# Optimization experiments

Measured on AMD Instinct MI355X. Metric: run time of the kernel, lower is better.

## Reference

```python
import jax, jax.numpy as jnp
import numpy as np

L, DIM, H, DH, MUL = 4, 1024, 16, 64, 4
INNER = H * DH
HID = DIM * MUL
EPS = 1e-5


def setup_inputs() -> dict:
    key = jax.random.key(0)
    ks = jax.random.split(key, 16)
    s = 0.02
    inp = {
        "x": jax.random.normal(ks[0], (2, 2048, DIM), dtype=jnp.float32),
        "ln1_g": jnp.ones((L, DIM), jnp.float32),
        "ln1_b": jnp.zeros((L, DIM), jnp.float32),
        "Wq": jax.random.normal(ks[1], (L, DIM, INNER), jnp.float32) * s,
        "Wk": jax.random.normal(ks[2], (L, DIM, INNER), jnp.float32) * s,
        "Wv": jax.random.normal(ks[3], (L, DIM, INNER), jnp.float32) * s,
        "Wo": jax.random.normal(ks[4], (L, INNER, DIM), jnp.float32) * s,
        "ln3_g": jnp.ones((L, DIM), jnp.float32),
        "ln3_b": jnp.zeros((L, DIM), jnp.float32),
        "fc1_w": jax.random.normal(ks[5], (L, DIM, HID), jnp.float32) * s,
        "fc1_b": jnp.zeros((L, HID), jnp.float32),
        "fc2_w": jax.random.normal(ks[6], (L, HID, DIM), jnp.float32) * s,
        "fc2_b": jnp.zeros((L, DIM), jnp.float32),
    }
    return inp


def _layernorm(x, g, b):
    mu = jnp.mean(x, axis=-1, keepdims=True)
    var = jnp.var(x, axis=-1, keepdims=True)
    return (x - mu) * jax.lax.rsqrt(var + EPS) * g + b


def _attention(xn, wq, wk, wv, wo):
    B, S, _ = xn.shape
    q = (xn @ wq).reshape(B, S, H, DH).transpose(0, 2, 1, 3)  # b h s d
    k = (xn @ wk).reshape(B, S, H, DH).transpose(0, 2, 1, 3)
    v = (xn @ wv).reshape(B, S, H, DH).transpose(0, 2, 1, 3)
    scale = DH ** -0.5
    sim = jnp.einsum("bhid,bhjd->bhij", q, k) * scale
    mask = jnp.triu(jnp.ones((S, S), dtype=bool), k=1)
    sim = jnp.where(mask, jnp.finfo(sim.dtype).min, sim)
    attn = jax.nn.softmax(sim, axis=-1)
    out = jnp.einsum("bhij,bhjd->bhid", attn, v)
    out = out.transpose(0, 2, 1, 3).reshape(B, S, INNER)
    return out @ wo


def reference(x, ln1_g, ln1_b, Wq, Wk, Wv, Wo, ln3_g, ln3_b, fc1_w, fc1_b, fc2_w, fc2_b):
    for l in range(L):
        x = x + _attention(_layernorm(x, ln1_g[l], ln1_b[l]), Wq[l], Wk[l], Wv[l], Wo[l])
        h = _layernorm(x, ln3_g[l], ln3_b[l])
        h = jax.nn.gelu(h @ fc1_w[l] + fc1_b[l], approximate=False)
        x = x + (h @ fc2_w[l] + fc2_b[l])
    return x
```

## Files before the change

### kernel.cpp

```cpp
#include <hip/hip_runtime.h>

typedef unsigned short u16;
typedef unsigned int u32;
typedef __attribute__((ext_vector_type(8))) short short8;
typedef __attribute__((ext_vector_type(4))) float f32x4;
typedef __attribute__((ext_vector_type(4))) unsigned short u16x4;

__device__ inline u16 f2bf(float f) {
  u32 u = __builtin_bit_cast(u32, f);
  u32 r = (u + 0x7fffu + ((u >> 16) & 1u)) >> 16;
  return (u16)r;
}

__device__ inline void gload16(const void* g, void* l) {
  __builtin_amdgcn_global_load_lds((const __attribute__((address_space(1))) void*)g,
                                   (__attribute__((address_space(3))) void*)l, 16, 0, 0);
}

__global__ __launch_bounds__(256) void transpose_cast(
    const float* __restrict__ src, u16* __restrict__ dst, int K, int N)
{
  __shared__ u16 tile[64][72];
  int bk = blockIdx.x * 64, bn = blockIdx.y * 64;
  int t = threadIdx.x;
  int r = t >> 2, c0 = (t & 3) * 16;
  const float* sp = src + (size_t)(bk + r) * N + bn + c0;
#pragma unroll
  for (int j = 0; j < 16; j += 4) {
    float4 v = *(const float4*)(sp + j);
    tile[r][c0 + j + 0] = f2bf(v.x);
    tile[r][c0 + j + 1] = f2bf(v.y);
    tile[r][c0 + j + 2] = f2bf(v.z);
    tile[r][c0 + j + 3] = f2bf(v.w);
  }
  __syncthreads();
  int nr = t >> 2, k0 = (t & 3) * 16;
  u16* dp = dst + (size_t)(bn + nr) * K + bk + k0;
  short8 v0, v1;
#pragma unroll
  for (int j = 0; j < 8; ++j) v0[j] = (short)tile[k0 + j][nr];
#pragma unroll
  for (int j = 0; j < 8; ++j) v1[j] = (short)tile[k0 + 8 + j][nr];
  *(short8*)dp = v0;
  *(short8*)(dp + 8) = v1;
}

__global__ __launch_bounds__(256) void vtranspose(
    const u16* __restrict__ qkv, u16* __restrict__ vtb)
{
  __shared__ u16 tile[64][72];
  int bt = blockIdx.x;
  int bh = blockIdx.y;
  int b = bh >> 4, h = bh & 15;
  const u16* src = qkv + (size_t)b * 2048 * 3072 + 2048 + h * 64;
  u16* dst = vtb + (size_t)bh * 64 * 2048;
  int t = threadIdx.x;
  int r = t >> 2, c0 = (t & 3) * 16;
  const u16* sp = src + (size_t)(bt * 64 + r) * 3072 + c0;
  *(short8*)&tile[r][c0] = *(const short8*)sp;
  *(short8*)&tile[r][c0 + 8] = *(const short8*)(sp + 8);
  __syncthreads();
  int nr = t >> 2, k0 = (t & 3) * 16;
  u16* dp = dst + (size_t)nr * 2048 + bt * 64 + k0;
  short8 v0, v1;
#pragma unroll
  for (int j = 0; j < 8; ++j) v0[j] = (short)tile[k0 + j][nr];
#pragma unroll
  for (int j = 0; j < 8; ++j) v1[j] = (short)tile[k0 + 8 + j][nr];
  *(short8*)dp = v0;
  *(short8*)(dp + 8) = v1;
}

__global__ __launch_bounds__(256) void ln_kernel(
    const float* __restrict__ x, const float* __restrict__ g,
    const float* __restrict__ be, u16* __restrict__ out)
{
  int row = blockIdx.x;
  int t = threadIdx.x;
  const float4* xr = (const float4*)(x + (size_t)row * 1024);
  float4 v = xr[t];
  float s = v.x + v.y + v.z + v.w;
  float ss = v.x * v.x + v.y * v.y + v.z * v.z + v.w * v.w;
#pragma unroll
  for (int off = 1; off < 64; off <<= 1) {
    s += __shfl_xor(s, off);
    ss += __shfl_xor(ss, off);
  }
  __shared__ float red[8];
  int w = t >> 6, lane = t & 63;
  if (lane == 0) { red[w * 2] = s; red[w * 2 + 1] = ss; }
  __syncthreads();
  s = red[0] + red[2] + red[4] + red[6];
  ss = red[1] + red[3] + red[5] + red[7];
  float mu = s * (1.0f / 1024.0f);
  float var = ss * (1.0f / 1024.0f) - mu * mu;
  float rs = rsqrtf(var + 1e-5f);
  float4 gg = ((const float4*)g)[t];
  float4 bb = ((const float4*)be)[t];
  u16x4 o;
  o[0] = f2bf((v.x - mu) * rs * gg.x + bb.x);
  o[1] = f2bf((v.y - mu) * rs * gg.y + bb.y);
  o[2] = f2bf((v.z - mu) * rs * gg.z + bb.z);
  o[3] = f2bf((v.w - mu) * rs * gg.w + bb.w);
  ((u16x4*)(out + (size_t)row * 1024))[t] = o;
}

template <int EPI, int BN>
__global__ __launch_bounds__(256) void gemm_bf16(
    const u16* __restrict__ A, const u16* __restrict__ Bt,
    u16* __restrict__ C, const float* __restrict__ bias, float* X,
    int M, int N, int K)
{
  constexpr int NJ = BN / 32;
  __shared__ __align__(16) u16 As[2][128 * 32];
  __shared__ __align__(16) u16 Bs[2][BN * 32];
  int bm = blockIdx.x * 128, bn = blockIdx.y * BN;
  int klen = K / gridDim.z;
  int kbeg = blockIdx.z * klen;
  int tid = threadIdx.x;
  int w = tid >> 6, lane = tid & 63;
  int wm = (w >> 1) * 64, wn = (w & 1) * (BN / 2);
  int frow = lane & 15, fkb = lane >> 4;

  f32x4 acc[4][NJ];
#pragma unroll
  for (int i = 0; i < 4; ++i)
#pragma unroll
    for (int j = 0; j < NJ; ++j) acc[i][j] = (f32x4){0.f, 0.f, 0.f, 0.f};

  int ca0 = tid, ca1 = tid + 256;
  int ar0 = ca0 >> 2, ak0 = (((ca0 & 3) ^ ((ar0 >> 1) & 3))) * 8;
  int ar1 = ca1 >> 2, ak1 = (((ca1 & 3) ^ ((ar1 >> 1) & 3))) * 8;
  const u16* Abase = A + (size_t)bm * K;
  const u16* Bbase = Bt + (size_t)bn * K;

  int offa[4], offb[NJ];
#pragma unroll
  for (int i = 0; i < 4; ++i) {
    int row = wm + i * 16 + frow;
    offa[i] = row * 32 + ((fkb ^ ((row >> 1) & 3)) * 8);
  }
#pragma unroll
  for (int j = 0; j < NJ; ++j) {
    int row = wn + j * 16 + frow;
    offb[j] = row * 32 + ((fkb ^ ((row >> 1) & 3)) * 8);
  }

  int nt = klen >> 5;

#define STAGE(buf, k0)                                                              \
  do {                                                                              \
    gload16(Abase + (size_t)ar0 * K + (k0) + ak0, &As[buf][(size_t)(w * 64) * 8]);  \
    gload16(Abase + (size_t)ar1 * K + (k0) + ak1, &As[buf][(size_t)(256 + w * 64) * 8]); \
    gload16(Bbase + (size_t)ar0 * K + (k0) + ak0, &Bs[buf][(size_t)(w * 64) * 8]);  \
    if constexpr (BN == 128)                                                        \
      gload16(Bbase + (size_t)ar1 * K + (k0) + ak1, &Bs[buf][(size_t)(256 + w * 64) * 8]); \
  } while (0)

  STAGE(0, kbeg);
  __syncthreads();
  int cur = 0;
  for (int t = 0; t < nt; ++t) {
    if (t + 1 < nt) STAGE(cur ^ 1, kbeg + (t + 1) * 32);
    short8 a[4], b[NJ];
#pragma unroll
    for (int i = 0; i < 4; ++i) a[i] = *(const short8*)&As[cur][offa[i]];
#pragma unroll
    for (int j = 0; j < NJ; ++j) b[j] = *(const short8*)&Bs[cur][offb[j]];
#pragma unroll
    for (int i = 0; i < 4; ++i)
#pragma unroll
      for (int j = 0; j < NJ; ++j)
        acc[i][j] = __builtin_amdgcn_mfma_f32_16x16x32_bf16(a[i], b[j], acc[i][j], 0, 0, 0);
    __syncthreads();
    cur ^= 1;
  }
#undef STAGE

  int r0 = (lane >> 4) * 4;
#pragma unroll
  for (int i = 0; i < 4; ++i) {
#pragma unroll
    for (int r = 0; r < 4; ++r) {
      int gr = bm + wm + i * 16 + r0 + r;
      size_t rowb = (size_t)gr * N;
#pragma unroll
      for (int j = 0; j < NJ; ++j) {
        int gc = bn + wn + j * 16 + frow;
        float v = acc[i][j][r];
        if constexpr (EPI == 0) {
          C[rowb + gc] = f2bf(v);
        } else if constexpr (EPI == 1) {
          v += bias[gc];
          v = 0.5f * v * (1.0f + erff(v * 0.70710678118654752f));
          C[rowb + gc] = f2bf(v);
        } else if constexpr (EPI == 2) {
          if (bias) v += bias[gc];
          X[rowb + gc] += v;
        } else {
          if (kbeg == 0 && bias) v += bias[gc];
          atomicAdd(&X[rowb + gc], v);
        }
      }
    }
  }
}

__global__ __launch_bounds__(256) void flash_attn4(
    const u16* __restrict__ qkv, const u16* __restrict__ vtb, u16* __restrict__ ao)
{
  const int SEQ = 2048, LDQ = 3072;
  const float SCL2 = 0.18033688011112042f;
  int ib = blockIdx.x;
  int qb = (ib < 256) ? (15 - (ib >> 5)) : ((ib - 256) >> 5);
  int bh = ib & 31;
  int b = bh >> 4, h = bh & 15;
  size_t base = (size_t)b * SEQ * LDQ;
  const u16* Qp = qkv + base + h * 64;
  const u16* Kp = qkv + base + 1024 + h * 64;
  const u16* Vtp = vtb + (size_t)bh * 64 * SEQ;

  __shared__ __align__(16) u16 Kt[64][72];
  __shared__ __align__(16) u16 Vt[64][72];
  __shared__ __align__(16) u16 Pl[4][32][72];

  int tid = threadIdx.x;
  int w = tid >> 6, lane = tid & 63;
  int frow = lane & 15, fkh = lane >> 4;
  int fk = fkh * 8;
  int qbase = qb * 128 + w * 32;

  short8 qf[2][2];
#pragma unroll
  for (int qi = 0; qi < 2; ++qi) {
    const u16* qr = Qp + (size_t)(qbase + qi * 16 + frow) * LDQ;
    qf[qi][0] = *(const short8*)(qr + fk);
    qf[qi][1] = *(const short8*)(qr + 32 + fk);
  }

  short8 ones;
#pragma unroll
  for (int j = 0; j < 8; ++j) ones[j] = (short)0x3F80;

  f32x4 o[2][4];
  f32x4 lacc[2];
#pragma unroll
  for (int qi = 0; qi < 2; ++qi) {
    lacc[qi] = (f32x4){0.f, 0.f, 0.f, 0.f};
#pragma unroll
    for (int nf = 0; nf < 4; ++nf) o[qi][nf] = (f32x4){0.f, 0.f, 0.f, 0.f};
  }

  int sr0 = tid >> 3, sc0 = (tid & 7) * 8;
  int sr1 = (tid + 256) >> 3, sc1 = ((tid + 256) & 7) * 8;

  int ntiles = qb * 2 + 2;

  short8 kr0 = *(const short8*)(Kp + (size_t)sr0 * LDQ + sc0);
  short8 kr1 = *(const short8*)(Kp + (size_t)sr1 * LDQ + sc1);
  short8 vr0 = *(const short8*)(Vtp + (size_t)sr0 * SEQ + sc0);
  short8 vr1 = *(const short8*)(Vtp + (size_t)sr1 * SEQ + sc1);

  for (int jb = 0; jb < ntiles; ++jb) {
    __syncthreads();
    *(short8*)&Kt[sr0][sc0] = kr0;
    *(short8*)&Kt[sr1][sc1] = kr1;
    *(short8*)&Vt[sr0][sc0] = vr0;
    *(short8*)&Vt[sr1][sc1] = vr1;
    __syncthreads();

    if (jb + 1 < ntiles) {
      kr0 = *(const short8*)(Kp + (size_t)((jb + 1) * 64 + sr0) * LDQ + sc0);
      kr1 = *(const short8*)(Kp + (size_t)((jb + 1) * 64 + sr1) * LDQ + sc1);
      vr0 = *(const short8*)(Vtp + (size_t)sr0 * SEQ + (jb + 1) * 64 + sc0);
      vr1 = *(const short8*)(Vtp + (size_t)sr1 * SEQ + (jb + 1) * 64 + sc1);
    }

    short8 kf[4][2];
#pragma unroll
    for (int nf = 0; nf < 4; ++nf) {
      kf[nf][0] = *(const short8*)&Kt[nf * 16 + frow][fk];
      kf[nf][1] = *(const short8*)&Kt[nf * 16 + frow][32 + fk];
    }

#pragma unroll
    for (int qi = 0; qi < 2; ++qi) {
      f32x4 s[4];
#pragma unroll
      for (int nf = 0; nf < 4; ++nf) s[nf] = (f32x4){0.f, 0.f, 0.f, 0.f};
#pragma unroll
      for (int nf = 0; nf < 4; ++nf) {
        s[nf] = __builtin_amdgcn_mfma_f32_16x16x32_bf16(qf[qi][0], kf[nf][0], s[nf], 0, 0, 0);
        s[nf] = __builtin_amdgcn_mfma_f32_16x16x32_bf16(qf[qi][1], kf[nf][1], s[nf], 0, 0, 0);
      }

      float pv[4][4];
#pragma unroll
      for (int nf = 0; nf < 4; ++nf)
#pragma unroll
        for (int r = 0; r < 4; ++r) pv[nf][r] = s[nf][r] * SCL2;

      bool needmask = (jb * 64 + 63) > (qbase + qi * 16);
      if (needmask) {
#pragma unroll
        for (int nf = 0; nf < 4; ++nf)
#pragma unroll
          for (int r = 0; r < 4; ++r) {
            int tok = jb * 64 + nf * 16 + frow;
            int qr = qbase + qi * 16 + fkh * 4 + r;
            if (tok > qr) pv[nf][r] = -1e30f;
          }
      }

#pragma unroll
      for (int nf = 0; nf < 4; ++nf)
#pragma unroll
        for (int r = 0; r < 4; ++r) {
          float p = exp2f(pv[nf][r]);
          Pl[w][qi * 16 + fkh * 4 + r][nf * 16 + frow] = f2bf(p);
        }
    }

    asm volatile("s_waitcnt lgkmcnt(0)" ::: "memory");
#pragma unroll
    for (int ks = 0; ks < 2; ++ks) {
      short8 pa0 = *(const short8*)&Pl[w][frow][ks * 32 + fk];
      short8 pa1 = *(const short8*)&Pl[w][16 + frow][ks * 32 + fk];
      lacc[0] = __builtin_amdgcn_mfma_f32_16x16x32_bf16(pa0, ones, lacc[0], 0, 0, 0);
      lacc[1] = __builtin_amdgcn_mfma_f32_16x16x32_bf16(pa1, ones, lacc[1], 0, 0, 0);
#pragma unroll
      for (int nf = 0; nf < 4; ++nf) {
        short8 vb = *(const short8*)&Vt[nf * 16 + frow][ks * 32 + fk];
        o[0][nf] = __builtin_amdgcn_mfma_f32_16x16x32_bf16(pa0, vb, o[0][nf], 0, 0, 0);
        o[1][nf] = __builtin_amdgcn_mfma_f32_16x16x32_bf16(pa1, vb, o[1][nf], 0, 0, 0);
      }
    }
  }

#pragma unroll
  for (int qi = 0; qi < 2; ++qi) {
#pragma unroll
    for (int nf = 0; nf < 4; ++nf) {
#pragma unroll
      for (int r = 0; r < 4; ++r) {
        int qr = qbase + qi * 16 + fkh * 4 + r;
        int dc = nf * 16 + frow;
        ao[((size_t)b * SEQ + qr) * 1024 + h * 64 + dc] = f2bf(o[qi][nf][r] / lacc[qi][r]);
      }
    }
  }
}

extern "C" void kernel_launch(void* const* d_in, const int* in_sizes, int n_in,
                              void* d_out, int out_size, void* d_ws, size_t ws_size,
                              hipStream_t stream)
{
  const float* x_in = (const float*)d_in[0];
  const float* ln1g = (const float*)d_in[1];
  const float* ln1b = (const float*)d_in[2];
  const float* Wq   = (const float*)d_in[3];
  const float* Wk   = (const float*)d_in[4];
  const float* Wv   = (const float*)d_in[5];
  const float* Wo   = (const float*)d_in[6];
  const float* ln3g = (const float*)d_in[7];
  const float* ln3b = (const float*)d_in[8];
  const float* fc1w = (const float*)d_in[9];
  const float* fc1b = (const float*)d_in[10];
  const float* fc2w = (const float*)d_in[11];
  const float* fc2b = (const float*)d_in[12];

  float* xbuf = (float*)d_out;

  char* ws = (char*)d_ws;
  size_t off = 0;
  u16* xn     = (u16*)(ws + off);  off += (size_t)4096 * 1024 * 2;
  u16* qkvb   = (u16*)(ws + off);  off += (size_t)4096 * 3072 * 2;
  u16* aob    = (u16*)(ws + off);  off += (size_t)4096 * 1024 * 2;
  u16* hbuf   = qkvb;
  u16* vtb    = (u16*)(ws + off);  off += (size_t)32 * 64 * 2048 * 2;
  u16* wqkv_l = (u16*)(ws + off);  off += (size_t)3072 * 1024 * 2;
  u16* wo_l   = (u16*)(ws + off);  off += (size_t)1024 * 1024 * 2;
  u16* wfc1_l = (u16*)(ws + off);  off += (size_t)4096 * 1024 * 2;
  u16* wfc2_l = (u16*)(ws + off);  off += (size_t)1024 * 4096 * 2;

  hipMemcpyAsync(xbuf, x_in, (size_t)4096 * 1024 * 4, hipMemcpyDeviceToDevice, stream);

  dim3 blk(256);
  for (int l = 0; l < 4; ++l) {
    transpose_cast<<<dim3(16, 16), blk, 0, stream>>>(Wq + (size_t)l * 1024 * 1024, wqkv_l,                        1024, 1024);
    transpose_cast<<<dim3(16, 16), blk, 0, stream>>>(Wk + (size_t)l * 1024 * 1024, wqkv_l + (size_t)1024 * 1024,  1024, 1024);
    transpose_cast<<<dim3(16, 16), blk, 0, stream>>>(Wv + (size_t)l * 1024 * 1024, wqkv_l + (size_t)2048 * 1024,  1024, 1024);
    transpose_cast<<<dim3(16, 16), blk, 0, stream>>>(Wo + (size_t)l * 1024 * 1024, wo_l,                          1024, 1024);
    transpose_cast<<<dim3(16, 64), blk, 0, stream>>>(fc1w + (size_t)l * 1024 * 4096, wfc1_l,                      1024, 4096);
    transpose_cast<<<dim3(64, 16), blk, 0, stream>>>(fc2w + (size_t)l * 4096 * 1024, wfc2_l,                      4096, 1024);

    ln_kernel<<<4096, blk, 0, stream>>>(xbuf, ln1g + l * 1024, ln1b + l * 1024, xn);
    gemm_bf16<0, 128><<<dim3(32, 24), blk, 0, stream>>>(xn, wqkv_l, qkvb, nullptr, nullptr, 4096, 3072, 1024);
    vtranspose<<<dim3(32, 32), blk, 0, stream>>>(qkvb, vtb);
    flash_attn4<<<dim3(512), blk, 0, stream>>>(qkvb, vtb, aob);
    gemm_bf16<3, 128><<<dim3(32, 8, 2), blk, 0, stream>>>(aob, wo_l, nullptr, nullptr, xbuf, 4096, 1024, 1024);
    ln_kernel<<<4096, blk, 0, stream>>>(xbuf, ln3g + l * 1024, ln3b + l * 1024, xn);
    gemm_bf16<1, 128><<<dim3(32, 32), blk, 0, stream>>>(xn, wfc1_l, hbuf, fc1b + l * 4096, nullptr, 4096, 4096, 1024);
    gemm_bf16<3, 128><<<dim3(32, 8, 4), blk, 0, stream>>>(hbuf, wfc2_l, nullptr, fc2b + l * 1024, xbuf, 4096, 1024, 4096);
  }
}
```

Before: 1.247 ms.

## Batch weight transposes across layers and retile Wo/fc2 GEMMs

Hoists the per-layer weight transpose-casts out of the layer loop into six launches that use blockIdx.z to cover all four layers, with full-size bf16 weight buffers for every layer. This cuts 24 small launches down to 6 and gives each launch a larger grid. The Wo projection changes from split-K atomic accumulation (mode 3, 128-wide tiles, K split 2) to a non-split mode 2 with 64-wide tiles. The fc2 GEMM moves to 64-wide tiles with K split 2 instead of 4. The workspace grows by roughly four times the weight storage, and it is assumed the mode-2 epilogue adds into xbuf as a residual.

Result: faster. 1.130 ms (-9.3%).

```diff
diff --git a/kernel.cpp b/kernel.cpp
--- a/kernel.cpp
+++ b/kernel.cpp
@@ -18,8 +18,11 @@
 }
 
 __global__ __launch_bounds__(256) void transpose_cast(
-    const float* __restrict__ src, u16* __restrict__ dst, int K, int N)
-{
+    const float* __restrict__ src, u16* __restrict__ dst, int K, int N,
+    size_t sstride, size_t dstride)
+{
+  src += (size_t)blockIdx.z * sstride;
+  dst += (size_t)blockIdx.z * dstride;
   __shared__ u16 tile[64][72];
   int bk = blockIdx.x * 64, bn = blockIdx.y * 64;
   int t = threadIdx.x;
@@ -378,29 +381,30 @@
   u16* aob    = (u16*)(ws + off);  off += (size_t)4096 * 1024 * 2;
   u16* hbuf   = qkvb;
   u16* vtb    = (u16*)(ws + off);  off += (size_t)32 * 64 * 2048 * 2;
-  u16* wqkv_l = (u16*)(ws + off);  off += (size_t)3072 * 1024 * 2;
-  u16* wo_l   = (u16*)(ws + off);  off += (size_t)1024 * 1024 * 2;
-  u16* wfc1_l = (u16*)(ws + off);  off += (size_t)4096 * 1024 * 2;
-  u16* wfc2_l = (u16*)(ws + off);  off += (size_t)1024 * 4096 * 2;
+  u16* wqkv   = (u16*)(ws + off);  off += (size_t)4 * 3072 * 1024 * 2;
+  u16* wo_t   = (u16*)(ws + off);  off += (size_t)4 * 1024 * 1024 * 2;
+  u16* wfc1   = (u16*)(ws + off);  off += (size_t)4 * 4096 * 1024 * 2;
+  u16* wfc2   = (u16*)(ws + off);  off += (size_t)4 * 1024 * 4096 * 2;
 
   hipMemcpyAsync(xbuf, x_in, (size_t)4096 * 1024 * 4, hipMemcpyDeviceToDevice, stream);
 
   dim3 blk(256);
+  const size_t W1 = (size_t)1024 * 1024;
+  transpose_cast<<<dim3(16, 16, 4), blk, 0, stream>>>(Wq, wqkv,                 1024, 1024, W1, (size_t)3072 * 1024);
+  transpose_cast<<<dim3(16, 16, 4), blk, 0, stream>>>(Wk, wqkv + W1,            1024, 1024, W1, (size_t)3072 * 1024);
+  transpose_cast<<<dim3(16, 16, 4), blk, 0, stream>>>(Wv, wqkv + 2 * W1,        1024, 1024, W1, (size_t)3072 * 1024);
+  transpose_cast<<<dim3(16, 16, 4), blk, 0, stream>>>(Wo, wo_t,                 1024, 1024, W1, W1);
+  transpose_cast<<<dim3(16, 64, 4), blk, 0, stream>>>(fc1w, wfc1,               1024, 4096, (size_t)4096 * 1024, (size_t)4096 * 1024);
+  transpose_cast<<<dim3(64, 16, 4), blk, 0, stream>>>(fc2w, wfc2,               4096, 1024, (size_t)4096 * 1024, (size_t)4096 * 1024);
+
   for (int l = 0; l < 4; ++l) {
-    transpose_cast<<<dim3(16, 16), blk, 0, stream>>>(Wq + (size_t)l * 1024 * 1024, wqkv_l,                        1024, 1024);
-    transpose_cast<<<dim3(16, 16), blk, 0, stream>>>(Wk + (size_t)l * 1024 * 1024, wqkv_l + (size_t)1024 * 1024,  1024, 1024);
-    transpose_cast<<<dim3(16, 16), blk, 0, stream>>>(Wv + (size_t)l * 1024 * 1024, wqkv_l + (size_t)2048 * 1024,  1024, 1024);
-    transpose_cast<<<dim3(16, 16), blk, 0, stream>>>(Wo + (size_t)l * 1024 * 1024, wo_l,                          1024, 1024);
-    transpose_cast<<<dim3(16, 64), blk, 0, stream>>>(fc1w + (size_t)l * 1024 * 4096, wfc1_l,                      1024, 4096);
-    transpose_cast<<<dim3(64, 16), blk, 0, stream>>>(fc2w + (size_t)l * 4096 * 1024, wfc2_l,                      4096, 1024);
-
     ln_kernel<<<4096, blk, 0, stream>>>(xbuf, ln1g + l * 1024, ln1b + l * 1024, xn);
-    gemm_bf16<0, 128><<<dim3(32, 24), blk, 0, stream>>>(xn, wqkv_l, qkvb, nullptr, nullptr, 4096, 3072, 1024);
+    gemm_bf16<0, 128><<<dim3(32, 24), blk, 0, stream>>>(xn, wqkv + (size_t)l * 3072 * 1024, qkvb, nullptr, nullptr, 4096, 3072, 1024);
     vtranspose<<<dim3(32, 32), blk, 0, stream>>>(qkvb, vtb);
     flash_attn4<<<dim3(512), blk, 0, stream>>>(qkvb, vtb, aob);
-    gemm_bf16<3, 128><<<dim3(32, 8, 2), blk, 0, stream>>>(aob, wo_l, nullptr, nullptr, xbuf, 4096, 1024, 1024);
+    gemm_bf16<2, 64><<<dim3(32, 16), blk, 0, stream>>>(aob, wo_t + (size_t)l * 1024 * 1024, nullptr, nullptr, xbuf, 4096, 1024, 1024);
     ln_kernel<<<4096, blk, 0, stream>>>(xbuf, ln3g + l * 1024, ln3b + l * 1024, xn);
-    gemm_bf16<1, 128><<<dim3(32, 32), blk, 0, stream>>>(xn, wfc1_l, hbuf, fc1b + l * 4096, nullptr, 4096, 4096, 1024);
-    gemm_bf16<3, 128><<<dim3(32, 8, 4), blk, 0, stream>>>(hbuf, wfc2_l, nullptr, fc2b + l * 1024, xbuf, 4096, 1024, 4096);
-  }
-}
+    gemm_bf16<1, 128><<<dim3(32, 32), blk, 0, stream>>>(xn, wfc1 + (size_t)l * 4096 * 1024, hbuf, fc1b + l * 4096, nullptr, 4096, 4096, 1024);
+    gemm_bf16<3, 64><<<dim3(32, 16, 2), blk, 0, stream>>>(hbuf, wfc2 + (size_t)l * 1024 * 4096, nullptr, fc2b + l * 1024, xbuf, 4096, 1024, 4096);
+  }
+}
```
